# Kernel optimization log

Hardware: AMD Instinct MI355X
Metric: run time of the kernel (lower is better)

## Reference

```python
import jax, jax.numpy as jnp
import numpy as np

D_MODEL = 1024
N_HEADS = 16
HEAD_DIM = D_MODEL // N_HEADS
WINDOW = 512


def _rope(q, k, seq_len, head_dim):
    # interleaved RoPE, identical to the torch implementation
    theta = 1.0 / 10000.0 ** (jnp.arange(0, head_dim, 2, dtype=jnp.float32) / head_dim)
    pos = jnp.arange(seq_len, dtype=jnp.float32)
    freqs = jnp.outer(pos, theta)                      # [S, hD/2]
    cos_f = jnp.cos(freqs)[None, None]                 # [1,1,S,hD/2]
    sin_f = jnp.sin(freqs)[None, None]

    def rotate(x):
        x1, x2 = x[..., ::2], x[..., 1::2]
        return jnp.stack([x1 * cos_f - x2 * sin_f, x1 * sin_f + x2 * cos_f], axis=-1).reshape(x.shape)

    return rotate(q), rotate(k)


def _sliding_window_attn(q, k, v, W, scale):
    # chunked O(S*W) causal sliding-window attention
    B, nH, S, hD = q.shape
    n_chunks = (S + W - 1) // W
    pad_s = n_chunks * W - S
    k_pad = jnp.pad(k, ((0, 0), (0, 0), (W, pad_s), (0, 0)))
    v_pad = jnp.pad(v, ((0, 0), (0, 0), (W, pad_s), (0, 0)))
    q_pad = jnp.pad(q, ((0, 0), (0, 0), (0, pad_s), (0, 0)))
    q_c = q_pad.reshape(B, nH, n_chunks, W, hD)
    k_r = k_pad.reshape(B, nH, n_chunks + 1, W, hD)
    v_r = v_pad.reshape(B, nH, n_chunks + 1, W, hD)
    # window i = chunks [i, i+1] of the left-padded sequence (== torch unfold)
    k_c = jnp.concatenate([k_r[:, :, :-1], k_r[:, :, 1:]], axis=3)  # [B,nH,C,2W,hD]
    v_c = jnp.concatenate([v_r[:, :, :-1], v_r[:, :, 1:]], axis=3)
    attn = jnp.einsum('bhcqd,bhckd->bhcqk', q_c, k_c) * scale

    qi = jnp.arange(W)[:, None]
    ki = jnp.arange(2 * W)[None, :]
    cw_mask = (ki <= qi) | (ki > qi + W)               # [W, 2W]
    chunk_idx = jnp.arange(n_chunks)[:, None]
    abs_k = chunk_idx * W + ki - W                     # [C, 2W]
    pad_mask = (abs_k < 0) | (abs_k >= S)
    q_pos = jnp.arange(n_chunks * W).reshape(n_chunks, W)
    full_mask = cw_mask[None] | pad_mask[:, None, :] | (q_pos >= S)[..., None]  # [C,W,2W]

    attn = jnp.where(full_mask[None, None], -jnp.inf, attn)
    attn = jax.nn.softmax(attn, axis=-1)
    attn = jnp.nan_to_num(attn, nan=0.0)
    out = jnp.einsum('bhcqk,bhckd->bhcqd', attn, v_c)
    return out.reshape(B, nH, n_chunks * W, hD)[:, :, :S]


def _rmsnorm(x, w):
    eps = jnp.finfo(x.dtype).eps
    return x * jax.lax.rsqrt(jnp.mean(x * x, axis=-1, keepdims=True) + eps) * w


def _sdpa(q, k, v, scale):
    s = jnp.einsum('bhqd,bhkd->bhqk', q, k) * scale
    return jnp.einsum('bhqk,bhkd->bhqd', jax.nn.softmax(s, axis=-1), v)


def setup_inputs() -> dict:
    key = jax.random.key(0)
    ks = jax.random.split(key, 11)
    D = D_MODEL
    std = 0.02
    return {
        'x': jax.random.normal(ks[0], (2, 4096, D), jnp.float32),
        'landmarks': jax.random.normal(ks[1], (2, 256, D), jnp.float32),
        'archived_landmarks': jax.random.normal(ks[2], (2, 128, D), jnp.float32),
        'W_qkv': jax.random.normal(ks[3], (D, 3 * D), jnp.float32) * std,
        'W_lm': jax.random.normal(ks[4], (D, 2 * D), jnp.float32) * std,
        'W_arch': jax.random.normal(ks[5], (D, 2 * D), jnp.float32) * std,
        'W_o': jax.random.normal(ks[6], (D, D), jnp.float32) * std,
        'W_gate': jax.random.normal(ks[7], (3 * D, 2 * D), jnp.float32) * std,
        'g_local': jnp.ones((D,), jnp.float32),
        'g_lm': jnp.ones((D,), jnp.float32),
        'g_arch': jnp.ones((D,), jnp.float32),
    }


def reference(x, landmarks, archived_landmarks, W_qkv, W_lm, W_arch, W_o, W_gate, g_local, g_lm, g_arch):
    B, S, D = x.shape
    nH, hD = N_HEADS, HEAD_DIM
    scale = hD ** -0.5

    def rsh(t, L):
        return jnp.transpose(t.reshape(B, L, nH, hD), (0, 2, 1, 3))

    q, k, v = jnp.split(x @ W_qkv, 3, axis=-1)
    Q, K, V = rsh(q, S), rsh(k, S), rsh(v, S)
    Q, K = _rope(Q, K, S, hD)

    Weff = min(WINDOW, S)
    out_loc = _sliding_window_attn(Q, K, V, Weff, scale)  # S > Weff -> chunked path
    out_loc = _rmsnorm(jnp.transpose(out_loc, (0, 2, 1, 3)).reshape(B, S, D), g_local)

    L = landmarks.shape[1]
    K_lm, V_lm = jnp.split(landmarks @ W_lm, 2, axis=-1)
    out_lm = _sdpa(Q, rsh(K_lm, L), rsh(V_lm, L), scale)
    out_lm = _rmsnorm(jnp.transpose(out_lm, (0, 2, 1, 3)).reshape(B, S, D), g_lm)

    A = archived_landmarks.shape[1]
    K_a, V_a = jnp.split(archived_landmarks @ W_arch, 2, axis=-1)
    out_a = _sdpa(Q, rsh(K_a, A), rsh(V_a, A), scale)
    out_a = _rmsnorm(jnp.transpose(out_a, (0, 2, 1, 3)).reshape(B, S, D), g_arch)

    concat = jnp.concatenate([out_loc, out_lm, out_a], axis=-1)
    gate, value = jnp.split(concat @ W_gate, 2, axis=-1)
    return (jax.nn.silu(gate) * value) @ W_o
```

## Files before the change

kernel.cpp:

```cpp
#include <hip/hip_runtime.h>
#include <cstdint>
#include <cstddef>

typedef __bf16 bf16;
typedef __bf16 bf16x2 __attribute__((ext_vector_type(2)));
typedef __bf16 bf16x4 __attribute__((ext_vector_type(4)));
typedef __bf16 bf16x8 __attribute__((ext_vector_type(8)));
typedef float  f32x2 __attribute__((ext_vector_type(2)));
typedef float  f32x4 __attribute__((ext_vector_type(4)));

#define DEVFN __device__ __forceinline__

DEVFN void gld_lds16(void* lds, const void* g) {
  __builtin_amdgcn_global_load_lds(
      (__attribute__((address_space(1))) void*)g,
      (__attribute__((address_space(3))) void*)lds,
      16, 0, 0);
}

__global__ void cast_f32_bf16(const float* __restrict__ in, bf16* __restrict__ out, int n4) {
  int i = blockIdx.x * blockDim.x + threadIdx.x;
  if (i < n4) {
    f32x4 v = reinterpret_cast<const f32x4*>(in)[i];
    bf16x4 o;
    o[0] = (bf16)v[0]; o[1] = (bf16)v[1]; o[2] = (bf16)v[2]; o[3] = (bf16)v[3];
    reinterpret_cast<bf16x4*>(out)[i] = o;
  }
}

__global__ void transpose_cast(const float* __restrict__ in, bf16* __restrict__ out,
                               int R, int C) {
  __shared__ float t[32][33];
  int tx = threadIdx.x, ty = threadIdx.y;
  int c = blockIdx.x * 32 + tx;
  #pragma unroll
  for (int j = 0; j < 4; ++j) {
    int r = blockIdx.y * 32 + ty + j * 8;
    t[ty + j * 8][tx] = in[(size_t)r * C + c];
  }
  __syncthreads();
  int rr = blockIdx.y * 32 + tx;
  #pragma unroll
  for (int j = 0; j < 4; ++j) {
    int cc = blockIdx.x * 32 + ty + j * 8;
    out[(size_t)cc * R + rr] = (bf16)t[tx][ty + j * 8];
  }
}

__global__ void rope_table(float* __restrict__ tab) {
  int idx = blockIdx.x * 256 + threadIdx.x;
  int s = idx >> 5, i = idx & 31;
  float theta = powf(10000.f, -(float)(2 * i) * (1.f / 64.f));
  float f = (float)s * theta;
  tab[idx * 2]     = cosf(f);
  tab[idx * 2 + 1] = sinf(f);
}

template<typename OT>
__global__ __launch_bounds__(256) void gemm_bf16(
    const bf16* __restrict__ A, const bf16* __restrict__ Bt, OT* __restrict__ C,
    int M, int N, int K) {
  __shared__ alignas(16) bf16 As[128 * 64];
  __shared__ alignas(16) bf16 Bs[128 * 64];
  int tid = threadIdx.x;
  int w = tid >> 6, l = tid & 63;
  int l15 = l & 15, lg = l >> 4;
  int m0 = blockIdx.y * 128;
  int n0 = blockIdx.x * 128;
  int wr = (w >> 1) * 64, wc = (w & 1) * 64;
  f32x4 acc[4][4] = {};
  const size_t aBase = (size_t)m0 * K;
  const size_t bBase = (size_t)n0 * K;
  int nk = K >> 6;
  for (int kt = 0; kt < nk; ++kt) {
    int k0 = kt << 6;
    #pragma unroll
    for (int it = 0; it < 4; ++it) {
      int c = it * 256 + tid;
      int row = c >> 3, c8 = c & 7;
      gld_lds16(&As[(size_t)(it * 256 + w * 64) * 8],
                A + aBase + (size_t)row * K + k0 + c8 * 8);
      gld_lds16(&Bs[(size_t)(it * 256 + w * 64) * 8],
                Bt + bBase + (size_t)row * K + k0 + c8 * 8);
    }
    __syncthreads();
    #pragma unroll
    for (int kk = 0; kk < 64; kk += 32) {
      bf16x8 a[4], b[4];
      #pragma unroll
      for (int i = 0; i < 4; ++i)
        a[i] = *reinterpret_cast<const bf16x8*>(&As[(wr + i * 16 + l15) * 64 + kk + lg * 8]);
      #pragma unroll
      for (int i = 0; i < 4; ++i)
        b[i] = *reinterpret_cast<const bf16x8*>(&Bs[(wc + i * 16 + l15) * 64 + kk + lg * 8]);
      #pragma unroll
      for (int mi = 0; mi < 4; ++mi)
        #pragma unroll
        for (int ni = 0; ni < 4; ++ni)
          acc[mi][ni] = __builtin_amdgcn_mfma_f32_16x16x32_bf16(a[mi], b[ni], acc[mi][ni], 0, 0, 0);
    }
    __syncthreads();
  }
  #pragma unroll
  for (int mi = 0; mi < 4; ++mi) {
    #pragma unroll
    for (int r = 0; r < 4; ++r) {
      int row = m0 + wr + mi * 16 + lg * 4 + r;
      OT* crow = C + (size_t)row * N + n0 + wc + l15;
      #pragma unroll
      for (int ni = 0; ni < 4; ++ni) crow[ni * 16] = (OT)acc[mi][ni][r];
    }
  }
}

__global__ void rope_qk(const bf16* __restrict__ qkv, const float* __restrict__ tab,
                        bf16* __restrict__ Qb, bf16* __restrict__ Kb) {
  int idx = blockIdx.x * 256 + threadIdx.x;
  int i = idx & 31;
  int h = (idx >> 5) & 15;
  int bs = idx >> 9;
  int s = bs & 4095;
  int b = bs >> 12;
  const bf16* row = qkv + (size_t)bs * 3072;
  bf16x2 q2 = *reinterpret_cast<const bf16x2*>(row + h * 64 + 2 * i);
  bf16x2 k2 = *reinterpret_cast<const bf16x2*>(row + 1024 + h * 64 + 2 * i);
  f32x2 cs = *reinterpret_cast<const f32x2*>(tab + s * 64 + 2 * i);
  float c = cs[0], sn = cs[1];
  float q0 = (float)q2[0], q1 = (float)q2[1];
  float k0 = (float)k2[0], k1 = (float)k2[1];
  size_t ob = (((size_t)(b * 16 + h) * 4096) + s) * 64 + 2 * i;
  bf16x2 qo, ko;
  qo[0] = (bf16)((q0 * c - q1 * sn) * 0.125f);
  qo[1] = (bf16)((q0 * sn + q1 * c) * 0.125f);
  ko[0] = (bf16)(k0 * c - k1 * sn);
  ko[1] = (bf16)(k0 * sn + k1 * c);
  *reinterpret_cast<bf16x2*>(Qb + ob) = qo;
  *reinterpret_cast<bf16x2*>(Kb + ob) = ko;
}

__global__ void kv_post(const bf16* __restrict__ kv, bf16* __restrict__ Kdst,
                        bf16* __restrict__ Vt, int Lk, int rs, int koff, int voff) {
  __shared__ float t[64][65];
  int s0 = blockIdx.x * 64;
  int h = blockIdx.y, b = blockIdx.z;
  int tid = threadIdx.x;
  int lane_d = tid & 63;
  int rq = tid >> 6;
  const bf16* base = kv + (size_t)b * Lk * rs;
  if (Kdst) {
    #pragma unroll
    for (int r = 0; r < 16; ++r) {
      int si = r * 4 + rq;
      Kdst[(((size_t)(b * 16 + h) * Lk) + s0 + si) * 64 + lane_d] =
          base[(size_t)(s0 + si) * rs + koff + h * 64 + lane_d];
    }
  }
  #pragma unroll
  for (int r = 0; r < 16; ++r) {
    int si = r * 4 + rq;
    t[si][lane_d] = (float)base[(size_t)(s0 + si) * rs + voff + h * 64 + lane_d];
  }
  __syncthreads();
  #pragma unroll
  for (int r = 0; r < 16; ++r) {
    int d = r * 4 + rq;
    Vt[(((size_t)(b * 16 + h) * 64) + d) * Lk + s0 + lane_d] = (bf16)t[lane_d][d];
  }
}

template<bool WINDOWED>
__global__ __launch_bounds__(256) void attn_kernel(
    const bf16* __restrict__ Qb, const bf16* __restrict__ Kb, const bf16* __restrict__ Vt,
    bf16* __restrict__ outc, int S, int Lk, int col_off) {
  __shared__ alignas(16) bf16 Ks[64 * 64];
  __shared__ alignas(16) bf16 Vs[64 * 64];
  __shared__ alignas(16) bf16 Ps[4][16 * 72];
  int tid = threadIdx.x;
  int w = tid >> 6, l = tid & 63;
  int l15 = l & 15, lg = l >> 4;
  int qt = blockIdx.x, h = blockIdx.y, b = blockIdx.z;

  size_t qrow = (((size_t)(b * 16 + h) * S) + qt * 64 + w * 16 + l15) * 64;
  bf16x8 qf[2];
  qf[0] = *reinterpret_cast<const bf16x8*>(Qb + qrow + lg * 8);
  qf[1] = *reinterpret_cast<const bf16x8*>(Qb + qrow + 32 + lg * 8);
  const bf16* Kbase = Kb + ((size_t)(b * 16 + h) * Lk) * 64;
  const bf16* Vbase = Vt + ((size_t)(b * 16 + h) * 64) * Lk;

  float mrow = -1e30f, lsum = 0.f;
  f32x4 acc[4] = {};

  int kt_hi, kt_lo;
  if (WINDOWED) { kt_hi = qt; kt_lo = qt >= 8 ? qt - 8 : 0; }
  else          { kt_hi = (Lk >> 6) - 1; kt_lo = 0; }

  for (int kt = kt_hi; kt >= kt_lo; --kt) {
    const bf16* kg = Kbase + (size_t)kt * 64 * 64;
    #pragma unroll
    for (int it = 0; it < 2; ++it)
      gld_lds16(&Ks[(it * 256 + w * 64) * 8], kg + (size_t)(it * 256 + tid) * 8);
    #pragma unroll
    for (int it = 0; it < 2; ++it) {
      int c = it * 256 + tid;
      int row = c >> 3, c8 = c & 7;
      gld_lds16(&Vs[(it * 256 + w * 64) * 8],
                Vbase + (size_t)row * Lk + kt * 64 + c8 * 8);
    }
    __syncthreads();

    f32x4 st[4] = {};
    #pragma unroll
    for (int kk = 0; kk < 2; ++kk) {
      #pragma unroll
      for (int f = 0; f < 4; ++f) {
        bf16x8 kf = *reinterpret_cast<const bf16x8*>(&Ks[(f * 16 + l15) * 64 + kk * 32 + lg * 8]);
        st[f] = __builtin_amdgcn_mfma_f32_16x16x32_bf16(kf, qf[kk], st[f], 0, 0, 0);
      }
    }

    if (WINDOWED) {
      int qi = w * 16 + l15;
      if (kt == qt) {
        #pragma unroll
        for (int f = 0; f < 4; ++f)
          #pragma unroll
          for (int r = 0; r < 4; ++r)
            if (f * 16 + lg * 4 + r > qi) st[f][r] = -1e30f;
      } else if (kt == qt - 8) {
        #pragma unroll
        for (int f = 0; f < 4; ++f)
          #pragma unroll
          for (int r = 0; r < 4; ++r)
            if (f * 16 + lg * 4 + r <= qi) st[f][r] = -1e30f;
      }
    }

    float rm = -1e30f;
    #pragma unroll
    for (int f = 0; f < 4; ++f)
      #pragma unroll
      for (int r = 0; r < 4; ++r) rm = fmaxf(rm, st[f][r]);
    rm = fmaxf(rm, __shfl_xor(rm, 16));
    rm = fmaxf(rm, __shfl_xor(rm, 32));
    float mnew = fmaxf(mrow, rm);
    float fsc = __expf(mrow - mnew);
    float ps = 0.f;
    bf16x4 pv[4];
    #pragma unroll
    for (int f = 0; f < 4; ++f)
      #pragma unroll
      for (int r = 0; r < 4; ++r) {
        float p = __expf(st[f][r] - mnew);
        ps += p;
        pv[f][r] = (bf16)p;
      }
    ps += __shfl_xor(ps, 16);
    ps += __shfl_xor(ps, 32);
    lsum = lsum * fsc + ps;
    mrow = mnew;

    #pragma unroll
    for (int f = 0; f < 4; ++f)
      *reinterpret_cast<bf16x4*>(&Ps[w][l15 * 72 + f * 16 + lg * 4]) = pv[f];

    #pragma unroll
    for (int r = 0; r < 4; ++r) {
      float fr = __shfl(fsc, lg * 4 + r);
      #pragma unroll
      for (int f = 0; f < 4; ++f) acc[f][r] *= fr;
    }

    #pragma unroll
    for (int kk = 0; kk < 2; ++kk) {
      bf16x8 pa = *reinterpret_cast<const bf16x8*>(&Ps[w][l15 * 72 + kk * 32 + lg * 8]);
      #pragma unroll
      for (int f = 0; f < 4; ++f) {
        bf16x8 vf = *reinterpret_cast<const bf16x8*>(&Vs[(f * 16 + l15) * 64 + kk * 32 + lg * 8]);
        acc[f] = __builtin_amdgcn_mfma_f32_16x16x32_bf16(pa, vf, acc[f], 0, 0, 0);
      }
    }
    __syncthreads();
  }

  float inv = 1.f / lsum;
  #pragma unroll
  for (int r = 0; r < 4; ++r) {
    float ir = __shfl(inv, lg * 4 + r);
    int srow = qt * 64 + w * 16 + lg * 4 + r;
    bf16* orow = outc + ((size_t)b * S + srow) * 3072 + col_off + h * 64 + l15;
    #pragma unroll
    for (int f = 0; f < 4; ++f) orow[f * 16] = (bf16)(acc[f][r] * ir);
  }
}

__global__ __launch_bounds__(256) void rmsnorm_kernel(
    bf16* data, const float* __restrict__ g0,
    const float* __restrict__ g1, const float* __restrict__ g2) {
  int token = blockIdx.x;
  int seg = blockIdx.y;
  const float* g = seg == 0 ? g0 : (seg == 1 ? g1 : g2);
  int tid = threadIdx.x;
  size_t base = (size_t)token * 3072 + seg * 1024;
  bf16x4 bv = reinterpret_cast<const bf16x4*>(data + base)[tid];
  f32x4 v;
  #pragma unroll
  for (int j = 0; j < 4; ++j) v[j] = (float)bv[j];
  float ss = v[0] * v[0] + v[1] * v[1] + v[2] * v[2] + v[3] * v[3];
  #pragma unroll
  for (int m = 1; m < 64; m <<= 1) ss += __shfl_xor(ss, m);
  __shared__ float red[4];
  if ((tid & 63) == 0) red[tid >> 6] = ss;
  __syncthreads();
  float tot = red[0] + red[1] + red[2] + red[3];
  float sc = rsqrtf(tot * (1.f / 1024.f) + 1.19209290e-07f);
  f32x4 gv = reinterpret_cast<const f32x4*>(g)[tid];
  bf16x4 o;
  #pragma unroll
  for (int j = 0; j < 4; ++j) o[j] = (bf16)(v[j] * sc * gv[j]);
  reinterpret_cast<bf16x4*>(data + base)[tid] = o;
}

__global__ void silu_kernel(const bf16* __restrict__ gv, bf16* __restrict__ out) {
  int T = blockIdx.x * 256 + threadIdx.x;
  int row = T >> 8, c4 = (T & 255) * 4;
  bf16x4 g = *reinterpret_cast<const bf16x4*>(gv + (size_t)row * 2048 + c4);
  bf16x4 vv = *reinterpret_cast<const bf16x4*>(gv + (size_t)row * 2048 + 1024 + c4);
  bf16x4 o;
  #pragma unroll
  for (int j = 0; j < 4; ++j) {
    float x = (float)g[j];
    o[j] = (bf16)((x / (1.f + __expf(-x))) * (float)vv[j]);
  }
  *reinterpret_cast<bf16x4*>(out + (size_t)row * 1024 + c4) = o;
}

extern "C" void kernel_launch(void* const* d_in, const int* in_sizes, int n_in,
                              void* d_out, int out_size, void* d_ws, size_t ws_size,
                              hipStream_t stream) {
  (void)in_sizes; (void)n_in; (void)out_size; (void)ws_size;
  const float* x       = (const float*)d_in[0];
  const float* lm      = (const float*)d_in[1];
  const float* arch    = (const float*)d_in[2];
  const float* W_qkv   = (const float*)d_in[3];
  const float* W_lm    = (const float*)d_in[4];
  const float* W_arch  = (const float*)d_in[5];
  const float* W_o     = (const float*)d_in[6];
  const float* W_gate  = (const float*)d_in[7];
  const float* g_local = (const float*)d_in[8];
  const float* g_lm    = (const float*)d_in[9];
  const float* g_arch  = (const float*)d_in[10];
  float* out = (float*)d_out;

  char* ws = (char*)d_ws;
  size_t off = 0;
  auto alloc = [&](size_t bytes) -> void* {
    void* p = ws + off;
    off += (bytes + 255) & ~(size_t)255;
    return p;
  };
  bf16*  Wqkv_t   = (bf16*) alloc(3072ull * 1024 * 2);
  bf16*  Wlm_t    = (bf16*) alloc(2048ull * 1024 * 2);
  bf16*  Warch_t  = (bf16*) alloc(2048ull * 1024 * 2);
  bf16*  Wgate_t  = (bf16*) alloc(2048ull * 3072 * 2);
  bf16*  Wo_t     = (bf16*) alloc(1024ull * 1024 * 2);
  bf16*  lm_bf    = (bf16*) alloc(512ull * 1024 * 2);
  bf16*  arch_bf  = (bf16*) alloc(256ull * 1024 * 2);
  float* ropetab  = (float*)alloc(4096ull * 64 * 4);
  bf16*  Klm      = (bf16*) alloc(2ull * 16 * 256 * 64 * 2);
  bf16*  Vlm_t    = (bf16*) alloc(2ull * 16 * 64 * 256 * 2);
  bf16*  Ka       = (bf16*) alloc(2ull * 16 * 128 * 64 * 2);
  bf16*  Va_t     = (bf16*) alloc(2ull * 16 * 64 * 128 * 2);
  bf16*  lmkv_bf  = (bf16*) alloc(512ull * 2048 * 2);
  bf16*  akv_bf   = (bf16*) alloc(256ull * 2048 * 2);
  char* R1 = (char*)alloc(8192ull * 1024 * 2);
  bf16* x_bf  = (bf16*)R1;
  bf16* gated = (bf16*)R1;
  char* R2 = (char*)alloc(8192ull * 3072 * 2);
  bf16* qkv_bf  = (bf16*)R2;
  bf16* concatb = (bf16*)R2;
  char* R3 = (char*)alloc(3ull * 16 * 1024 * 1024);
  bf16* Qb = (bf16*)R3;
  bf16* Kb = (bf16*)(R3 + 16ull * 1024 * 1024);
  bf16* Vt = (bf16*)(R3 + 32ull * 1024 * 1024);
  bf16* gv = (bf16*)R3;

  transpose_cast<<<dim3(96, 32), dim3(32, 8), 0, stream>>>(W_qkv, Wqkv_t, 1024, 3072);
  transpose_cast<<<dim3(64, 32), dim3(32, 8), 0, stream>>>(W_lm, Wlm_t, 1024, 2048);
  transpose_cast<<<dim3(64, 32), dim3(32, 8), 0, stream>>>(W_arch, Warch_t, 1024, 2048);
  transpose_cast<<<dim3(64, 96), dim3(32, 8), 0, stream>>>(W_gate, Wgate_t, 3072, 2048);
  transpose_cast<<<dim3(32, 32), dim3(32, 8), 0, stream>>>(W_o, Wo_t, 1024, 1024);
  cast_f32_bf16<<<8192, 256, 0, stream>>>(x, x_bf, 8192 * 1024 / 4);
  cast_f32_bf16<<<512, 256, 0, stream>>>(lm, lm_bf, 512 * 1024 / 4);
  cast_f32_bf16<<<256, 256, 0, stream>>>(arch, arch_bf, 256 * 1024 / 4);
  rope_table<<<512, 256, 0, stream>>>(ropetab);

  gemm_bf16<bf16><<<dim3(24, 64), 256, 0, stream>>>(x_bf, Wqkv_t, qkv_bf, 8192, 3072, 1024);
  gemm_bf16<bf16><<<dim3(16, 4), 256, 0, stream>>>(lm_bf, Wlm_t, lmkv_bf, 512, 2048, 1024);
  gemm_bf16<bf16><<<dim3(16, 2), 256, 0, stream>>>(arch_bf, Warch_t, akv_bf, 256, 2048, 1024);

  rope_qk<<<16384, 256, 0, stream>>>(qkv_bf, ropetab, Qb, Kb);
  kv_post<<<dim3(64, 16, 2), 256, 0, stream>>>(qkv_bf, nullptr, Vt, 4096, 3072, 0, 2048);
  kv_post<<<dim3(4, 16, 2), 256, 0, stream>>>(lmkv_bf, Klm, Vlm_t, 256, 2048, 0, 1024);
  kv_post<<<dim3(2, 16, 2), 256, 0, stream>>>(akv_bf, Ka, Va_t, 128, 2048, 0, 1024);

  attn_kernel<true><<<dim3(64, 16, 2), 256, 0, stream>>>(Qb, Kb, Vt, concatb, 4096, 4096, 0);
  attn_kernel<false><<<dim3(64, 16, 2), 256, 0, stream>>>(Qb, Klm, Vlm_t, concatb, 4096, 256, 1024);
  attn_kernel<false><<<dim3(64, 16, 2), 256, 0, stream>>>(Qb, Ka, Va_t, concatb, 4096, 128, 2048);

  rmsnorm_kernel<<<dim3(8192, 3), 256, 0, stream>>>(concatb, g_local, g_lm, g_arch);

  gemm_bf16<bf16><<<dim3(16, 64), 256, 0, stream>>>(concatb, Wgate_t, gv, 8192, 2048, 3072);
  silu_kernel<<<8192, 256, 0, stream>>>(gv, gated);
  gemm_bf16<float><<<dim3(8, 64), 256, 0, stream>>>(gated, Wo_t, out, 8192, 1024, 1024);
}
```

Before: 490.1 us.

## Double-buffer GEMMs with swizzled LDS, fuse SiLU into gate GEMM, split-K landmark projections

Replaces the GEMM with a templated double-buffered kernel. It prefetches the next 32-wide K slice while issuing MFMAs, uses an XOR-swizzled LDS layout to cut bank conflicts, remaps workgroups for L2 locality and raises MFMA priority. The gate GEMM computes the gate and value halves together and applies SiLU in its epilogue, so the separate silu kernel and its intermediate buffer go away. The small landmark projections switch to 4-way split-K with fp32 partials that a new kv_post4 kernel reduces. Attention K/V tiles also get XOR-swizzled LDS addressing. The trade-offs are larger register pressure in the fused GEMM and extra fp32 partial traffic for split-K.

```diff
diff --git a/kernel.cpp b/kernel.cpp
--- a/kernel.cpp
+++ b/kernel.cpp
@@ -10,6 +10,8 @@
 typedef float  f32x4 __attribute__((ext_vector_type(4)));
 
 #define DEVFN __device__ __forceinline__
+#define BAR()  asm volatile("s_barrier" ::: "memory")
+#define VMW0() asm volatile("s_waitcnt vmcnt(0)" ::: "memory")
 
 DEVFN void gld_lds16(void* lds, const void* g) {
   __builtin_amdgcn_global_load_lds(
@@ -56,59 +58,113 @@
   tab[idx * 2 + 1] = sinf(f);
 }
 
-template<typename OT>
-__global__ __launch_bounds__(256) void gemm_bf16(
+template<int BM, bool FUSE, typename OT>
+__global__ __launch_bounds__(BM * 2) void gemmT(
     const bf16* __restrict__ A, const bf16* __restrict__ Bt, OT* __restrict__ C,
-    int M, int N, int K) {
-  __shared__ alignas(16) bf16 As[128 * 64];
-  __shared__ alignas(16) bf16 Bs[128 * 64];
-  int tid = threadIdx.x;
-  int w = tid >> 6, l = tid & 63;
-  int l15 = l & 15, lg = l >> 4;
-  int m0 = blockIdx.y * 128;
-  int n0 = blockIdx.x * 128;
-  int wr = (w >> 1) * 64, wc = (w & 1) * 64;
-  f32x4 acc[4][4] = {};
-  const size_t aBase = (size_t)m0 * K;
-  const size_t bBase = (size_t)n0 * K;
-  int nk = K >> 6;
-  for (int kt = 0; kt < nk; ++kt) {
-    int k0 = kt << 6;
-    #pragma unroll
-    for (int it = 0; it < 4; ++it) {
-      int c = it * 256 + tid;
-      int row = c >> 3, c8 = c & 7;
-      gld_lds16(&As[(size_t)(it * 256 + w * 64) * 8],
-                A + aBase + (size_t)row * K + k0 + c8 * 8);
-      gld_lds16(&Bs[(size_t)(it * 256 + w * 64) * 8],
-                Bt + bBase + (size_t)row * K + k0 + c8 * 8);
-    }
-    __syncthreads();
-    #pragma unroll
-    for (int kk = 0; kk < 64; kk += 32) {
-      bf16x8 a[4], b[4];
-      #pragma unroll
-      for (int i = 0; i < 4; ++i)
-        a[i] = *reinterpret_cast<const bf16x8*>(&As[(wr + i * 16 + l15) * 64 + kk + lg * 8]);
-      #pragma unroll
-      for (int i = 0; i < 4; ++i)
-        b[i] = *reinterpret_cast<const bf16x8*>(&Bs[(wc + i * 16 + l15) * 64 + kk + lg * 8]);
+    int Nout, int Kc, int lda, long long skstride) {
+  constexpr int BR   = FUSE ? 256 : 128;
+  constexpr int NT   = BM * 2;
+  constexpr int AISS = (BM * 4) / NT;
+  constexpr int BISS = (BR * 4) / NT;
+  __shared__ alignas(16) bf16 ldsA[2][BM * 32];
+  __shared__ alignas(16) bf16 ldsB[2][BR * 32];
+  const int tid = threadIdx.x;
+  const int w = tid >> 6, l = tid & 63;
+  const int l15 = l & 15, lg = l >> 4;
+  const int wm = w >> 1, wn = w & 1;
+  const int nwg = gridDim.x, qx = nwg >> 3;
+  const int swz = (blockIdx.x & 7) * qx + (blockIdx.x >> 3);
+  const int gx = Nout >> 7;
+  const int m0 = (swz / gx) * BM;
+  const int n0 = (swz % gx) << 7;
+  const int sk = blockIdx.y;
+  A  += (size_t)sk * Kc;
+  Bt += (size_t)sk * Kc;
+  C  += (size_t)sk * skstride;
+
+  auto stage = [&](int buf, int s) {
+    const int kcol = s << 5;
+    #pragma unroll
+    for (int i = 0; i < AISS; ++i) {
+      int u = i * NT + tid;
+      int row = u >> 2, slot = u & 3;
+      int ss = slot ^ ((row >> 1) & 3);
+      gld_lds16(&ldsA[buf][(i * NT + w * 64) * 8],
+                A + (size_t)(m0 + row) * lda + kcol + ss * 8);
+    }
+    #pragma unroll
+    for (int i = 0; i < BISS; ++i) {
+      int u = i * NT + tid;
+      int row = u >> 2, slot = u & 3;
+      int ss = slot ^ ((row >> 1) & 3);
+      int srow = FUSE ? (n0 + row + ((row >> 7) * 896)) : (n0 + row);
+      gld_lds16(&ldsB[buf][(i * NT + w * 64) * 8],
+                Bt + (size_t)srow * lda + kcol + ss * 8);
+    }
+  };
+  auto rdA = [&](int buf, int r) -> bf16x8 {
+    return *reinterpret_cast<const bf16x8*>(
+        &ldsA[buf][(r << 5) + ((lg ^ ((r >> 1) & 3)) << 3)]);
+  };
+  auto rdB = [&](int buf, int r) -> bf16x8 {
+    return *reinterpret_cast<const bf16x8*>(
+        &ldsB[buf][(r << 5) + ((lg ^ ((r >> 1) & 3)) << 3)]);
+  };
+
+  f32x4 acc0[4][4] = {};
+  f32x4 acc1[4][4] = {};
+
+  stage(0, 0);
+  VMW0();
+  BAR();
+
+  const int ns = Kc >> 5;
+  for (int s = 0; s < ns; ++s) {
+    const int b = s & 1;
+    bf16x8 af[4], bf0[4], bf1[4];
+    #pragma unroll
+    for (int f = 0; f < 4; ++f) af[f]  = rdA(b, wm * 64 + f * 16 + l15);
+    #pragma unroll
+    for (int f = 0; f < 4; ++f) bf0[f] = rdB(b, wn * 64 + f * 16 + l15);
+    if constexpr (FUSE) {
+      #pragma unroll
+      for (int f = 0; f < 4; ++f) bf1[f] = rdB(b, 128 + wn * 64 + f * 16 + l15);
+    }
+    if (s + 1 < ns) stage(b ^ 1, s + 1);
+    __builtin_amdgcn_s_setprio(1);
+    #pragma unroll
+    for (int mi = 0; mi < 4; ++mi)
+      #pragma unroll
+      for (int ni = 0; ni < 4; ++ni)
+        acc0[mi][ni] = __builtin_amdgcn_mfma_f32_16x16x32_bf16(af[mi], bf0[ni], acc0[mi][ni], 0, 0, 0);
+    if constexpr (FUSE) {
       #pragma unroll
       for (int mi = 0; mi < 4; ++mi)
         #pragma unroll
         for (int ni = 0; ni < 4; ++ni)
-          acc[mi][ni] = __builtin_amdgcn_mfma_f32_16x16x32_bf16(a[mi], b[ni], acc[mi][ni], 0, 0, 0);
-    }
-    __syncthreads();
-  }
+          acc1[mi][ni] = __builtin_amdgcn_mfma_f32_16x16x32_bf16(af[mi], bf1[ni], acc1[mi][ni], 0, 0, 0);
+    }
+    __builtin_amdgcn_s_setprio(0);
+    VMW0();
+    BAR();
+  }
+
   #pragma unroll
   for (int mi = 0; mi < 4; ++mi) {
     #pragma unroll
     for (int r = 0; r < 4; ++r) {
-      int row = m0 + wr + mi * 16 + lg * 4 + r;
-      OT* crow = C + (size_t)row * N + n0 + wc + l15;
-      #pragma unroll
-      for (int ni = 0; ni < 4; ++ni) crow[ni * 16] = (OT)acc[mi][ni][r];
+      int row = m0 + wm * 64 + mi * 16 + lg * 4 + r;
+      OT* crow = C + (size_t)row * Nout + n0 + wn * 64 + l15;
+      if constexpr (FUSE) {
+        #pragma unroll
+        for (int ni = 0; ni < 4; ++ni) {
+          float g = acc0[mi][ni][r], v = acc1[mi][ni][r];
+          crow[ni * 16] = (OT)((g / (1.f + __expf(-g))) * v);
+        }
+      } else {
+        #pragma unroll
+        for (int ni = 0; ni < 4; ++ni) crow[ni * 16] = (OT)acc0[mi][ni][r];
+      }
     }
   }
 }
@@ -168,6 +224,34 @@
   }
 }
 
+__global__ void kv_post4(const float* __restrict__ kv, bf16* __restrict__ Kdst,
+                         bf16* __restrict__ Vt, int Lk, int Mtot) {
+  __shared__ float t[64][65];
+  int s0 = blockIdx.x * 64;
+  int h = blockIdx.y, b = blockIdx.z;
+  int tid = threadIdx.x;
+  int lane_d = tid & 63;
+  int rq = tid >> 6;
+  const size_t slab = (size_t)Mtot * 2048;
+  const float* base = kv + (size_t)b * Lk * 2048;
+  #pragma unroll
+  for (int r = 0; r < 16; ++r) {
+    int si = r * 4 + rq;
+    size_t o = (size_t)(s0 + si) * 2048 + h * 64 + lane_d;
+    float kvv = base[o] + base[slab + o] + base[2 * slab + o] + base[3 * slab + o];
+    size_t ov = o + 1024;
+    float vvv = base[ov] + base[slab + ov] + base[2 * slab + ov] + base[3 * slab + ov];
+    Kdst[(((size_t)(b * 16 + h) * Lk) + s0 + si) * 64 + lane_d] = (bf16)kvv;
+    t[si][lane_d] = vvv;
+  }
+  __syncthreads();
+  #pragma unroll
+  for (int r = 0; r < 16; ++r) {
+    int d = r * 4 + rq;
+    Vt[(((size_t)(b * 16 + h) * 64) + d) * Lk + s0 + lane_d] = (bf16)t[lane_d][d];
+  }
+}
+
 template<bool WINDOWED>
 __global__ __launch_bounds__(256) void attn_kernel(
     const bf16* __restrict__ Qb, const bf16* __restrict__ Kb, const bf16* __restrict__ Vt,
@@ -197,14 +281,17 @@
   for (int kt = kt_hi; kt >= kt_lo; --kt) {
     const bf16* kg = Kbase + (size_t)kt * 64 * 64;
     #pragma unroll
-    for (int it = 0; it < 2; ++it)
-      gld_lds16(&Ks[(it * 256 + w * 64) * 8], kg + (size_t)(it * 256 + tid) * 8);
-    #pragma unroll
     for (int it = 0; it < 2; ++it) {
-      int c = it * 256 + tid;
-      int row = c >> 3, c8 = c & 7;
+      int u = it * 256 + tid;
+      int row = u >> 3, sl = u & 7;
+      gld_lds16(&Ks[(it * 256 + w * 64) * 8], kg + row * 64 + (sl ^ (row & 7)) * 8);
+    }
+    #pragma unroll
+    for (int it = 0; it < 2; ++it) {
+      int u = it * 256 + tid;
+      int row = u >> 3, sl = u & 7;
       gld_lds16(&Vs[(it * 256 + w * 64) * 8],
-                Vbase + (size_t)row * Lk + kt * 64 + c8 * 8);
+                Vbase + (size_t)row * Lk + kt * 64 + (sl ^ (row & 7)) * 8);
     }
     __syncthreads();
 
@@ -213,7 +300,8 @@
     for (int kk = 0; kk < 2; ++kk) {
       #pragma unroll
       for (int f = 0; f < 4; ++f) {
-        bf16x8 kf = *reinterpret_cast<const bf16x8*>(&Ks[(f * 16 + l15) * 64 + kk * 32 + lg * 8]);
+        bf16x8 kf = *reinterpret_cast<const bf16x8*>(
+            &Ks[(f * 16 + l15) * 64 + (((kk * 4 + lg) ^ (l15 & 7)) << 3)]);
         st[f] = __builtin_amdgcn_mfma_f32_16x16x32_bf16(kf, qf[kk], st[f], 0, 0, 0);
       }
     }
@@ -275,7 +363,8 @@
       bf16x8 pa = *reinterpret_cast<const bf16x8*>(&Ps[w][l15 * 72 + kk * 32 + lg * 8]);
       #pragma unroll
       for (int f = 0; f < 4; ++f) {
-        bf16x8 vf = *reinterpret_cast<const bf16x8*>(&Vs[(f * 16 + l15) * 64 + kk * 32 + lg * 8]);
+        bf16x8 vf = *reinterpret_cast<const bf16x8*>(
+            &Vs[(f * 16 + l15) * 64 + (((kk * 4 + lg) ^ (l15 & 7)) << 3)]);
         acc[f] = __builtin_amdgcn_mfma_f32_16x16x32_bf16(pa, vf, acc[f], 0, 0, 0);
       }
     }
@@ -318,20 +407,6 @@
   #pragma unroll
   for (int j = 0; j < 4; ++j) o[j] = (bf16)(v[j] * sc * gv[j]);
   reinterpret_cast<bf16x4*>(data + base)[tid] = o;
-}
-
-__global__ void silu_kernel(const bf16* __restrict__ gv, bf16* __restrict__ out) {
-  int T = blockIdx.x * 256 + threadIdx.x;
-  int row = T >> 8, c4 = (T & 255) * 4;
-  bf16x4 g = *reinterpret_cast<const bf16x4*>(gv + (size_t)row * 2048 + c4);
-  bf16x4 vv = *reinterpret_cast<const bf16x4*>(gv + (size_t)row * 2048 + 1024 + c4);
-  bf16x4 o;
-  #pragma unroll
-  for (int j = 0; j < 4; ++j) {
-    float x = (float)g[j];
-    o[j] = (bf16)((x / (1.f + __expf(-x))) * (float)vv[j]);
-  }
-  *reinterpret_cast<bf16x4*>(out + (size_t)row * 1024 + c4) = o;
 }
 
 extern "C" void kernel_launch(void* const* d_in, const int* in_sizes, int n_in,
@@ -370,11 +445,11 @@
   bf16*  Vlm_t    = (bf16*) alloc(2ull * 16 * 64 * 256 * 2);
   bf16*  Ka       = (bf16*) alloc(2ull * 16 * 128 * 64 * 2);
   bf16*  Va_t     = (bf16*) alloc(2ull * 16 * 64 * 128 * 2);
-  bf16*  lmkv_bf  = (bf16*) alloc(512ull * 2048 * 2);
-  bf16*  akv_bf   = (bf16*) alloc(256ull * 2048 * 2);
-  char* R1 = (char*)alloc(8192ull * 1024 * 2);
-  bf16* x_bf  = (bf16*)R1;
-  bf16* gated = (bf16*)R1;
+  char* R1 = (char*)alloc(24ull * 1024 * 1024);
+  bf16*  x_bf   = (bf16*)R1;
+  float* lmP    = (float*)R1;
+  float* archP  = (float*)(R1 + 16ull * 1024 * 1024);
+  bf16*  gated  = (bf16*)R1;
   char* R2 = (char*)alloc(8192ull * 3072 * 2);
   bf16* qkv_bf  = (bf16*)R2;
   bf16* concatb = (bf16*)R2;
@@ -382,7 +457,6 @@
   bf16* Qb = (bf16*)R3;
   bf16* Kb = (bf16*)(R3 + 16ull * 1024 * 1024);
   bf16* Vt = (bf16*)(R3 + 32ull * 1024 * 1024);
-  bf16* gv = (bf16*)R3;
 
   transpose_cast<<<dim3(96, 32), dim3(32, 8), 0, stream>>>(W_qkv, Wqkv_t, 1024, 3072);
   transpose_cast<<<dim3(64, 32), dim3(32, 8), 0, stream>>>(W_lm, Wlm_t, 1024, 2048);
@@ -394,14 +468,17 @@
   cast_f32_bf16<<<256, 256, 0, stream>>>(arch, arch_bf, 256 * 1024 / 4);
   rope_table<<<512, 256, 0, stream>>>(ropetab);
 
-  gemm_bf16<bf16><<<dim3(24, 64), 256, 0, stream>>>(x_bf, Wqkv_t, qkv_bf, 8192, 3072, 1024);
-  gemm_bf16<bf16><<<dim3(16, 4), 256, 0, stream>>>(lm_bf, Wlm_t, lmkv_bf, 512, 2048, 1024);
-  gemm_bf16<bf16><<<dim3(16, 2), 256, 0, stream>>>(arch_bf, Warch_t, akv_bf, 256, 2048, 1024);
+  gemmT<256, false, bf16><<<dim3(768, 1), 512, 0, stream>>>(
+      x_bf, Wqkv_t, qkv_bf, 3072, 1024, 1024, 0);
+  gemmT<128, false, float><<<dim3(64, 4), 256, 0, stream>>>(
+      lm_bf, Wlm_t, lmP, 2048, 256, 1024, 512ll * 2048);
+  gemmT<128, false, float><<<dim3(32, 4), 256, 0, stream>>>(
+      arch_bf, Warch_t, archP, 2048, 256, 1024, 256ll * 2048);
 
   rope_qk<<<16384, 256, 0, stream>>>(qkv_bf, ropetab, Qb, Kb);
   kv_post<<<dim3(64, 16, 2), 256, 0, stream>>>(qkv_bf, nullptr, Vt, 4096, 3072, 0, 2048);
-  kv_post<<<dim3(4, 16, 2), 256, 0, stream>>>(lmkv_bf, Klm, Vlm_t, 256, 2048, 0, 1024);
-  kv_post<<<dim3(2, 16, 2), 256, 0, stream>>>(akv_bf, Ka, Va_t, 128, 2048, 0, 1024);
+  kv_post4<<<dim3(4, 16, 2), 256, 0, stream>>>(lmP, Klm, Vlm_t, 256, 512);
+  kv_post4<<<dim3(2, 16, 2), 256, 0, stream>>>(archP, Ka, Va_t, 128, 256);
 
   attn_kernel<true><<<dim3(64, 16, 2), 256, 0, stream>>>(Qb, Kb, Vt, concatb, 4096, 4096, 0);
   attn_kernel<false><<<dim3(64, 16, 2), 256, 0, stream>>>(Qb, Klm, Vlm_t, concatb, 4096, 256, 1024);
@@ -409,7 +486,8 @@
 
   rmsnorm_kernel<<<dim3(8192, 3), 256, 0, stream>>>(concatb, g_local, g_lm, g_arch);
 
-  gemm_bf16<bf16><<<dim3(16, 64), 256, 0, stream>>>(concatb, Wgate_t, gv, 8192, 2048, 3072);
-  silu_kernel<<<8192, 256, 0, stream>>>(gv, gated);
-  gemm_bf16<float><<<dim3(8, 64), 256, 0, stream>>>(gated, Wo_t, out, 8192, 1024, 1024);
-}
+  gemmT<128, true, bf16><<<dim3(512, 1), 256, 0, stream>>>(
+      concatb, Wgate_t, gated, 1024, 3072, 3072, 0);
+  gemmT<128, false, float><<<dim3(512, 1), 256, 0, stream>>>(
+      gated, Wo_t, out, 1024, 1024, 1024, 0);
+}
```

Result: faster. 469.1 us (-4.3%).
